# Optimization experiments

Hardware: AMD Instinct MI355X
Metric: run time of the kernel (lower is better)

## Reference

```python
import jax, jax.numpy as jnp
import numpy as np
from jax import lax

B, K, SF, BORDER = 2, 512, 8, 10
H, W = 256, 256
C1, C2 = 64, 128
C = C1 + C2  # feature_channels -> DescMatchingModule in_channels
OUT_CH = 2


def setup_inputs() -> dict:
    key = jax.random.key(0)
    ks = jax.random.split(key, 8)
    return {
        "heatmaps1": jax.random.normal(ks[0], (B, 1, H, W), jnp.float32),
        "heatmaps2": jax.random.normal(ks[1], (B, 1, H, W), jnp.float32),
        "feat1a": jax.random.normal(ks[2], (B, C1, H, W), jnp.float32),
        "feat1b": jax.random.normal(ks[3], (B, C2, H // 2, W // 2), jnp.float32),
        "feat2a": jax.random.normal(ks[4], (B, C1, H, W), jnp.float32),
        "feat2b": jax.random.normal(ks[5], (B, C2, H // 2, W // 2), jnp.float32),
        "fc_w": jax.random.normal(ks[6], (OUT_CH, C), jnp.float32) * np.sqrt(2.0 / C),
        "fc_b": jnp.zeros((OUT_CH,), jnp.float32),
    }


def bilinear_sample(img, gx, gy):
    # img: [b,c,h,w]; gx,gy: [b,k] normalized coords in [-1,1] (align_corners=True)
    b, c, h, w = img.shape
    ix = (gx + 1.0) * 0.5 * (w - 1)
    iy = (gy + 1.0) * 0.5 * (h - 1)
    x0 = jnp.floor(ix); y0 = jnp.floor(iy)
    wx = (ix - x0)[:, None, :]
    wy = (iy - y0)[:, None, :]

    def gather(xx, yy):
        xx = jnp.clip(xx.astype(jnp.int32), 0, w - 1)
        yy = jnp.clip(yy.astype(jnp.int32), 0, h - 1)
        return jax.vmap(lambda im, y_, x_: im[:, y_, x_])(img, yy, xx)  # [b,c,k]

    v00 = gather(x0, y0); v01 = gather(x0 + 1, y0)
    v10 = gather(x0, y0 + 1); v11 = gather(x0 + 1, y0 + 1)
    return (v00 * (1 - wx) * (1 - wy) + v01 * wx * (1 - wy)
            + v10 * (1 - wx) * wy + v11 * wx * wy)  # [b,c,k]


def sampling_layer(heatmap_logits, feats):
    # heatmap_logits: [b,1,H,W]; feats: list of [b,ci,hi,wi]
    b = heatmap_logits.shape[0]
    h = jax.nn.sigmoid(heatmap_logits)
    # max_pool2d + max_unpool2d NMS: keep only window maxima, zero elsewhere
    pooled = lax.reduce_window(h, -jnp.inf, lax.max,
                               (1, 1, SF, SF), (1, 1, SF, SF), 'VALID')
    up = jnp.repeat(jnp.repeat(pooled, SF, axis=2), SF, axis=3)
    nms = jnp.where(h >= up, h, 0.0)
    # border mask
    mask = jnp.zeros((H, W), h.dtype).at[BORDER:H - BORDER, BORDER:W - BORDER].set(1.0)
    nms = nms * mask
    # top-k keypoints by NMS score (training path: always take k points)
    flat = nms.reshape(b, H * W)
    _, idx = lax.top_k(flat, K)            # [b,K]
    row = (idx // W).astype(jnp.float32)   # y (image row)
    col = (idx % W).astype(jnp.float32)    # x (image col)
    gx = 2.0 * col / (W - 1) - 1.0
    gy = 2.0 * row / (H - 1) - 1.0
    pts = jnp.stack([gx, gy], axis=-1)[:, :, None, :]  # [b,K,1,2]
    score = bilinear_sample(h, gx, gy)[:, 0, :]        # [b,K], from sigmoid heatmap
    desc = jnp.concatenate([bilinear_sample(f, gx, gy) for f in feats], axis=1)  # [b,C,K]
    return pts, score, desc


def desc_matching(d1, d2, fc_w, fc_b):
    # d1,d2: [b,C,K] -> [b,K,C]
    o1 = jnp.transpose(d1, (0, 2, 1))
    o2 = jnp.transpose(d2, (0, 2, 1))
    b, k1, c = o1.shape
    k2 = o2.shape[1]
    prod = o1[:, :, None, :] * o2[:, None, :, :]               # [b,k1,k2,C]
    out = prod.reshape(-1, c) @ fc_w.T + fc_b                  # [b*k1*k2, 2]
    n1 = o1 / (1e-6 + jnp.linalg.norm(o1, axis=-1, keepdims=True))
    n2 = o2 / (1e-6 + jnp.linalg.norm(o2, axis=-1, keepdims=True))
    diff = n1[:, :, None, :] - n2[:, None, :, :]
    out_norm = jnp.linalg.norm(diff, axis=-1)                  # [b,k1,k2]
    return out, out_norm


def reference(heatmaps1, heatmaps2, feat1a, feat1b, feat2a, feat2b, fc_w, fc_b):
    lm1, probs1, desc1 = sampling_layer(heatmaps1, [feat1a, feat1b])
    lm2, probs2, desc2 = sampling_layer(heatmaps2, [feat2a, feat2b])
    score, norm = desc_matching(desc1, desc2, fc_w, fc_b)
    return (probs1, probs2, lm1, lm2, score, norm)
```

## Files before the change

kernel.cpp:

```cpp
#include <hip/hip_runtime.h>
#include <hip/hip_bf16.h>
#include <math.h>

#define NPIX 65536

typedef short short8 __attribute__((ext_vector_type(8)));
typedef float f32x4 __attribute__((ext_vector_type(4)));

__device__ int            g_kp_idx[2048];
__device__ float          g_invws[2048];
__device__ float          g_nnws[2048];
__device__ __hip_bfloat16 g_dbf[2048 * 192];
__device__ __hip_bfloat16 g_dw0[1024 * 192];
__device__ __hip_bfloat16 g_dw1[1024 * 192];

__device__ __forceinline__ unsigned long long u64min(unsigned long long a, unsigned long long b) {
    return a < b ? a : b;
}
__device__ __forceinline__ unsigned long long u64max(unsigned long long a, unsigned long long b) {
    return a > b ? a : b;
}

__global__ __launch_bounds__(1024) void nms_topk_kernel(
        const float* __restrict__ hm1, const float* __restrict__ hm2,
        float* __restrict__ out) {
    __shared__ unsigned long long keys[1024];
    int img = blockIdx.x;
    int t = threadIdx.x;
    int b = img & 1, hmid = img >> 1;
    const float* hp = (hmid ? hm2 : hm1) + b * NPIX;

    int wy = t >> 5, wx = t & 31;
    const float* wp = hp + wy * 8 * 256 + wx * 8;
    float mv = -3.4e38f;
    int mi = 0;
    #pragma unroll
    for (int r = 0; r < 8; ++r) {
        float4 v0 = *reinterpret_cast<const float4*>(wp + r * 256);
        float4 v1 = *reinterpret_cast<const float4*>(wp + r * 256 + 4);
        float s[8] = {v0.x, v0.y, v0.z, v0.w, v1.x, v1.y, v1.z, v1.w};
        int rowbase = (wy * 8 + r) * 256 + wx * 8;
        #pragma unroll
        for (int cidx = 0; cidx < 8; ++cidx) {
            if (s[cidx] > mv) { mv = s[cidx]; mi = rowbase + cidx; }
        }
    }
    int ay = mi >> 8, ax = mi & 255;
    bool interior = (ay >= 10 && ay < 246 && ax >= 10 && ax < 246);
    unsigned int ub = __float_as_uint(mv);
    unsigned int mk = (ub & 0x80000000u) ? ~ub : (ub | 0x80000000u);
    if (!interior) mk = 0u;
    unsigned long long k = ((unsigned long long)(~mk) << 32) |
                           (unsigned long long)(unsigned int)mi;

    for (int size = 2; size <= 1024; size <<= 1) {
        for (int stride = size >> 1; stride >= 1; stride >>= 1) {
            bool dir_up = ((t & size) == 0);
            unsigned long long pk;
            if (stride >= 64) {
                __syncthreads();
                keys[t] = k;
                __syncthreads();
                pk = keys[t ^ stride];
            } else {
                pk = __shfl_xor(k, stride);
            }
            bool low = ((t & stride) == 0);
            k = ((low == dir_up)) ? u64min(k, pk) : u64max(k, pk);
        }
    }

    if (t < 512) {
        unsigned int fidx = (unsigned int)(k & 0xFFFFFFFFull);
        unsigned int mk2 = ~(unsigned int)(k >> 32);
        unsigned int lb = (mk2 & 0x80000000u) ? (mk2 ^ 0x80000000u) : ~mk2;
        float logit = __uint_as_float(lb);
        float v = 1.0f / (1.0f + expf(-logit));
        int row = fidx >> 8, col = fidx & 255;
        float gx = 2.0f * (float)col / 255.0f - 1.0f;
        float gy = 2.0f * (float)row / 255.0f - 1.0f;
        out[hmid * 1024 + b * 512 + t] = v;
        float* lm = out + (hmid ? 4096 : 2048) + (size_t)(b * 512 + t) * 2;
        lm[0] = gx; lm[1] = gy;
        g_kp_idx[img * 512 + t] = (int)fidx;
    }
}

__global__ __launch_bounds__(256) void desc_kernel(
        const float* __restrict__ f1a, const float* __restrict__ f1b,
        const float* __restrict__ f2a, const float* __restrict__ f2b,
        const float* __restrict__ fcw) {
    int wave = threadIdx.x >> 6, lane = threadIdx.x & 63;
    int kp = blockIdx.x * 4 + wave;
    int img = kp >> 9, b = img & 1, hmid = img >> 1;
    int fidx = g_kp_idx[kp];
    int row = fidx >> 8, col = fidx & 255;

    const float* fa = (hmid ? f2a : f1a) + (size_t)(b * 64 + lane) * 65536;
    float vfa = fa[fidx];

    float gx = 2.0f * (float)col / 255.0f - 1.0f;
    float gy = 2.0f * (float)row / 255.0f - 1.0f;
    float ix = (gx + 1.0f) * 0.5f * 127.0f;
    float iy = (gy + 1.0f) * 0.5f * 127.0f;
    int x0 = (int)ix, y0 = (int)iy;
    float wx = ix - (float)x0, wy = iy - (float)y0;
    float w00 = (1 - wx) * (1 - wy), w01 = wx * (1 - wy);
    float w10 = (1 - wx) * wy,       w11 = wx * wy;

    const float* fb0 = (hmid ? f2b : f1b) + (size_t)(b * 128 + lane) * 16384
                       + y0 * 128 + x0;
    float vb1 = fb0[0] * w00 + fb0[1] * w01 + fb0[128] * w10 + fb0[129] * w11;
    const float* fb1 = fb0 + (size_t)64 * 16384;
    float vb2 = fb1[0] * w00 + fb1[1] * w01 + fb1[128] * w10 + fb1[129] * w11;

    __hip_bfloat16* dp = g_dbf + (size_t)kp * 192;
    dp[lane]       = __float2bfloat16(vfa);
    dp[lane + 64]  = __float2bfloat16(vb1);
    dp[lane + 128] = __float2bfloat16(vb2);

    if (kp < 1024) {
        __hip_bfloat16* q0 = g_dw0 + (size_t)kp * 192;
        __hip_bfloat16* q1 = g_dw1 + (size_t)kp * 192;
        q0[lane]       = __float2bfloat16(vfa * fcw[lane]);
        q0[lane + 64]  = __float2bfloat16(vb1 * fcw[lane + 64]);
        q0[lane + 128] = __float2bfloat16(vb2 * fcw[lane + 128]);
        q1[lane]       = __float2bfloat16(vfa * fcw[192 + lane]);
        q1[lane + 64]  = __float2bfloat16(vb1 * fcw[192 + lane + 64]);
        q1[lane + 128] = __float2bfloat16(vb2 * fcw[192 + lane + 128]);
    }

    float sq = vfa * vfa + vb1 * vb1 + vb2 * vb2;
    #pragma unroll
    for (int m = 1; m <= 32; m <<= 1) sq += __shfl_xor(sq, m);
    if (lane == 0) {
        float nrm = sqrtf(sq);
        float inv = 1.0f / (1e-6f + nrm);
        g_invws[kp] = inv;
        g_nnws[kp] = sq * inv * inv;
    }
}

__global__ __launch_bounds__(256) void match_kernel(
        const float* __restrict__ fcb, float* __restrict__ out) {
    int t = threadIdx.x;
    int w = t >> 6, lane = t & 63;
    int b = blockIdx.z;
    int k1base = blockIdx.y * 16;
    int k2base = blockIdx.x * 64 + w * 16;
    int r1 = k1base + (lane & 15);
    int r2 = k2base + (lane & 15);
    int koff = (lane >> 4) * 8;

    const __hip_bfloat16* pA  = g_dbf + (size_t)(b * 512 + r1) * 192 + koff;
    const __hip_bfloat16* pW0 = g_dw0 + (size_t)(b * 512 + r1) * 192 + koff;
    const __hip_bfloat16* pW1 = g_dw1 + (size_t)(b * 512 + r1) * 192 + koff;
    const __hip_bfloat16* pB  = g_dbf + (size_t)((2 + b) * 512 + r2) * 192 + koff;

    f32x4 accd = {0.f, 0.f, 0.f, 0.f};
    f32x4 acc0 = {0.f, 0.f, 0.f, 0.f};
    f32x4 acc1 = {0.f, 0.f, 0.f, 0.f};
    #pragma unroll
    for (int kc = 0; kc < 6; ++kc) {
        short8 a  = *reinterpret_cast<const short8*>(pA  + kc * 32);
        short8 a0 = *reinterpret_cast<const short8*>(pW0 + kc * 32);
        short8 a1 = *reinterpret_cast<const short8*>(pW1 + kc * 32);
        short8 bb = *reinterpret_cast<const short8*>(pB  + kc * 32);
        accd = __builtin_amdgcn_mfma_f32_16x16x32_bf16(a,  bb, accd, 0, 0, 0);
        acc0 = __builtin_amdgcn_mfma_f32_16x16x32_bf16(a0, bb, acc0, 0, 0, 0);
        acc1 = __builtin_amdgcn_mfma_f32_16x16x32_bf16(a1, bb, acc1, 0, 0, 0);
    }

    float bb0 = fcb[0], bb1 = fcb[1];
    int col = lane & 15;
    int k2 = k2base + col;
    float inv2 = g_invws[(2 + b) * 512 + k2];
    float nn2  = g_nnws[(2 + b) * 512 + k2];
    #pragma unroll
    for (int j = 0; j < 4; ++j) {
        int k1 = k1base + (lane >> 4) * 4 + j;
        float inv1 = g_invws[b * 512 + k1];
        float nn1  = g_nnws[b * 512 + k1];
        size_t sidx = (size_t)(b * 512 + k1) * 512 + k2;
        float2 sc = make_float2(acc0[j] + bb0, acc1[j] + bb1);
        *reinterpret_cast<float2*>(out + 6144 + sidx * 2) = sc;
        float arg = nn1 + nn2 - 2.0f * inv1 * inv2 * accd[j];
        out[1054720 + sidx] = sqrtf(fmaxf(arg, 0.0f));
    }
}

extern "C" void kernel_launch(void* const* d_in, const int* in_sizes, int n_in,
                              void* d_out, int out_size, void* d_ws, size_t ws_size,
                              hipStream_t stream) {
    const float* hm1 = (const float*)d_in[0];
    const float* hm2 = (const float*)d_in[1];
    const float* f1a = (const float*)d_in[2];
    const float* f1b = (const float*)d_in[3];
    const float* f2a = (const float*)d_in[4];
    const float* f2b = (const float*)d_in[5];
    const float* fcw = (const float*)d_in[6];
    const float* fcb = (const float*)d_in[7];
    float* out = (float*)d_out;
    (void)d_ws; (void)ws_size;

    nms_topk_kernel<<<4, 1024, 0, stream>>>(hm1, hm2, out);
    desc_kernel<<<512, 256, 0, stream>>>(f1a, f1b, f2a, f2b, fcw);
    dim3 g(8, 32, 2);
    match_kernel<<<g, 256, 0, stream>>>(fcb, out);
}
```

Measured before the change: 39.44 us.

## Split NMS window max into wide kernel and spread descriptor sampling across blocks

The window-max step moves out of the four-block top-k kernel into its own 1024-block kernel, with one wave per 8x8 window and a shuffle reduction. The candidates are staged in a global buffer for a separate bitonic top-k kernel. The descriptor kernel now uses one 192-thread block per keypoint, one thread per channel, with a shared-memory partial norm reduction. The goal is more parallelism for the heatmap scan and the gathers, at the cost of an extra kernel launch and a global round trip for the candidates.

```diff
diff --git a/kernel.cpp b/kernel.cpp
--- a/kernel.cpp
+++ b/kernel.cpp
@@ -7,6 +7,7 @@
 typedef short short8 __attribute__((ext_vector_type(8)));
 typedef float f32x4 __attribute__((ext_vector_type(4)));
 
+__device__ unsigned long long g_cand[4096];
 __device__ int            g_kp_idx[2048];
 __device__ float          g_invws[2048];
 __device__ float          g_nnws[2048];
@@ -21,37 +22,43 @@
     return a > b ? a : b;
 }
 
-__global__ __launch_bounds__(1024) void nms_topk_kernel(
-        const float* __restrict__ hm1, const float* __restrict__ hm2,
-        float* __restrict__ out) {
+__global__ __launch_bounds__(256) void winmax_kernel(
+        const float* __restrict__ hm1, const float* __restrict__ hm2) {
+    int wid  = blockIdx.x * 4 + (threadIdx.x >> 6);
+    int lane = threadIdx.x & 63;
+    int img  = wid >> 10;
+    int win  = wid & 1023;
+    int b = img & 1;
+    const float* hp = ((img >> 1) ? hm2 : hm1) + b * NPIX;
+    int wy = win >> 5, wx = win & 31;
+    int py = wy * 8 + (lane >> 3);
+    int px = wx * 8 + (lane & 7);
+    int fidx = py * 256 + px;
+    float mv = hp[fidx];
+    int mi = fidx;
+    #pragma unroll
+    for (int m = 1; m <= 32; m <<= 1) {
+        float ov = __shfl_xor(mv, m);
+        int   oi = __shfl_xor(mi, m);
+        if (ov > mv || (ov == mv && oi < mi)) { mv = ov; mi = oi; }
+    }
+    if (lane == 0) {
+        int ay = mi >> 8, ax = mi & 255;
+        bool interior = (ay >= 10 && ay < 246 && ax >= 10 && ax < 246);
+        unsigned int ub = __float_as_uint(mv);
+        unsigned int mk = (ub & 0x80000000u) ? ~ub : (ub | 0x80000000u);
+        if (!interior) mk = 0u;
+        g_cand[wid] = ((unsigned long long)(~mk) << 32) |
+                      (unsigned long long)(unsigned int)mi;
+    }
+}
+
+__global__ __launch_bounds__(1024) void topk_kernel(float* __restrict__ out) {
     __shared__ unsigned long long keys[1024];
     int img = blockIdx.x;
     int t = threadIdx.x;
     int b = img & 1, hmid = img >> 1;
-    const float* hp = (hmid ? hm2 : hm1) + b * NPIX;
-
-    int wy = t >> 5, wx = t & 31;
-    const float* wp = hp + wy * 8 * 256 + wx * 8;
-    float mv = -3.4e38f;
-    int mi = 0;
-    #pragma unroll
-    for (int r = 0; r < 8; ++r) {
-        float4 v0 = *reinterpret_cast<const float4*>(wp + r * 256);
-        float4 v1 = *reinterpret_cast<const float4*>(wp + r * 256 + 4);
-        float s[8] = {v0.x, v0.y, v0.z, v0.w, v1.x, v1.y, v1.z, v1.w};
-        int rowbase = (wy * 8 + r) * 256 + wx * 8;
-        #pragma unroll
-        for (int cidx = 0; cidx < 8; ++cidx) {
-            if (s[cidx] > mv) { mv = s[cidx]; mi = rowbase + cidx; }
-        }
-    }
-    int ay = mi >> 8, ax = mi & 255;
-    bool interior = (ay >= 10 && ay < 246 && ax >= 10 && ax < 246);
-    unsigned int ub = __float_as_uint(mv);
-    unsigned int mk = (ub & 0x80000000u) ? ~ub : (ub | 0x80000000u);
-    if (!interior) mk = 0u;
-    unsigned long long k = ((unsigned long long)(~mk) << 32) |
-                           (unsigned long long)(unsigned int)mi;
+    unsigned long long k = g_cand[img * 1024 + t];
 
     for (int size = 2; size <= 1024; size <<= 1) {
         for (int stride = size >> 1; stride >= 1; stride >>= 1) {
@@ -86,58 +93,52 @@
     }
 }
 
-__global__ __launch_bounds__(256) void desc_kernel(
+__global__ void desc_kernel(
         const float* __restrict__ f1a, const float* __restrict__ f1b,
         const float* __restrict__ f2a, const float* __restrict__ f2b,
         const float* __restrict__ fcw) {
-    int wave = threadIdx.x >> 6, lane = threadIdx.x & 63;
-    int kp = blockIdx.x * 4 + wave;
+    __shared__ float part[3];
+    int kp = blockIdx.x;
+    int c = threadIdx.x;
     int img = kp >> 9, b = img & 1, hmid = img >> 1;
     int fidx = g_kp_idx[kp];
     int row = fidx >> 8, col = fidx & 255;
 
-    const float* fa = (hmid ? f2a : f1a) + (size_t)(b * 64 + lane) * 65536;
-    float vfa = fa[fidx];
-
-    float gx = 2.0f * (float)col / 255.0f - 1.0f;
-    float gy = 2.0f * (float)row / 255.0f - 1.0f;
-    float ix = (gx + 1.0f) * 0.5f * 127.0f;
-    float iy = (gy + 1.0f) * 0.5f * 127.0f;
-    int x0 = (int)ix, y0 = (int)iy;
-    float wx = ix - (float)x0, wy = iy - (float)y0;
-    float w00 = (1 - wx) * (1 - wy), w01 = wx * (1 - wy);
-    float w10 = (1 - wx) * wy,       w11 = wx * wy;
-
-    const float* fb0 = (hmid ? f2b : f1b) + (size_t)(b * 128 + lane) * 16384
-                       + y0 * 128 + x0;
-    float vb1 = fb0[0] * w00 + fb0[1] * w01 + fb0[128] * w10 + fb0[129] * w11;
-    const float* fb1 = fb0 + (size_t)64 * 16384;
-    float vb2 = fb1[0] * w00 + fb1[1] * w01 + fb1[128] * w10 + fb1[129] * w11;
-
-    __hip_bfloat16* dp = g_dbf + (size_t)kp * 192;
-    dp[lane]       = __float2bfloat16(vfa);
-    dp[lane + 64]  = __float2bfloat16(vb1);
-    dp[lane + 128] = __float2bfloat16(vb2);
-
+    float val;
+    if (c < 64) {
+        const float* fa = (hmid ? f2a : f1a) + (size_t)(b * 64 + c) * 65536;
+        val = fa[fidx];
+    } else {
+        float gx = 2.0f * (float)col / 255.0f - 1.0f;
+        float gy = 2.0f * (float)row / 255.0f - 1.0f;
+        float ix = (gx + 1.0f) * 0.5f * 127.0f;
+        float iy = (gy + 1.0f) * 0.5f * 127.0f;
+        int x0 = (int)ix, y0 = (int)iy;
+        float wx = ix - (float)x0, wy = iy - (float)y0;
+        const float* fb0 = (hmid ? f2b : f1b) + (size_t)(b * 128 + (c - 64)) * 16384
+                           + y0 * 128 + x0;
+        float v00 = fb0[0], v01 = fb0[1], v10 = fb0[128], v11 = fb0[129];
+        val = v00 * (1 - wx) * (1 - wy) + v01 * wx * (1 - wy)
+            + v10 * (1 - wx) * wy       + v11 * wx * wy;
+    }
+
+    g_dbf[(size_t)kp * 192 + c] = __float2bfloat16(val);
     if (kp < 1024) {
-        __hip_bfloat16* q0 = g_dw0 + (size_t)kp * 192;
-        __hip_bfloat16* q1 = g_dw1 + (size_t)kp * 192;
-        q0[lane]       = __float2bfloat16(vfa * fcw[lane]);
-        q0[lane + 64]  = __float2bfloat16(vb1 * fcw[lane + 64]);
-        q0[lane + 128] = __float2bfloat16(vb2 * fcw[lane + 128]);
-        q1[lane]       = __float2bfloat16(vfa * fcw[192 + lane]);
-        q1[lane + 64]  = __float2bfloat16(vb1 * fcw[192 + lane + 64]);
-        q1[lane + 128] = __float2bfloat16(vb2 * fcw[192 + lane + 128]);
-    }
-
-    float sq = vfa * vfa + vb1 * vb1 + vb2 * vb2;
+        g_dw0[(size_t)kp * 192 + c] = __float2bfloat16(val * fcw[c]);
+        g_dw1[(size_t)kp * 192 + c] = __float2bfloat16(val * fcw[192 + c]);
+    }
+
+    float sq = val * val;
     #pragma unroll
     for (int m = 1; m <= 32; m <<= 1) sq += __shfl_xor(sq, m);
-    if (lane == 0) {
-        float nrm = sqrtf(sq);
+    if ((threadIdx.x & 63) == 0) part[threadIdx.x >> 6] = sq;
+    __syncthreads();
+    if (threadIdx.x == 0) {
+        float ss = part[0] + part[1] + part[2];
+        float nrm = sqrtf(ss);
         float inv = 1.0f / (1e-6f + nrm);
         g_invws[kp] = inv;
-        g_nnws[kp] = sq * inv * inv;
+        g_nnws[kp] = ss * inv * inv;
     }
 }
 
@@ -172,8 +173,8 @@
     }
 
     float bb0 = fcb[0], bb1 = fcb[1];
-    int col = lane & 15;
-    int k2 = k2base + col;
+    int colc = lane & 15;
+    int k2 = k2base + colc;
     float inv2 = g_invws[(2 + b) * 512 + k2];
     float nn2  = g_nnws[(2 + b) * 512 + k2];
     #pragma unroll
@@ -203,8 +204,9 @@
     float* out = (float*)d_out;
     (void)d_ws; (void)ws_size;
 
-    nms_topk_kernel<<<4, 1024, 0, stream>>>(hm1, hm2, out);
-    desc_kernel<<<512, 256, 0, stream>>>(f1a, f1b, f2a, f2b, fcw);
+    winmax_kernel<<<1024, 256, 0, stream>>>(hm1, hm2);
+    topk_kernel<<<4, 1024, 0, stream>>>(out);
+    desc_kernel<<<2048, 192, 0, stream>>>(f1a, f1b, f2a, f2b, fcw);
     dim3 g(8, 32, 2);
     match_kernel<<<g, 256, 0, stream>>>(fcb, out);
 }
```

After: 40.93 us. 1.04x slower.

## Stage half-res feature channels in LDS and compute norms in match kernel

Applied to the files above, without the earlier changes.

The descriptor kernel is split into two block roles. Even blocks load one full 128x128 half-resolution channel into shared memory (64 KB) and bilinearly sample all 512 keypoints from it. Odd blocks gather the full-resolution channel values per keypoint. Descriptor norms are no longer computed there: the match kernel recomputes them from the bf16 descriptors into shared memory, so the per-row global norm arrays go away. The aim is to replace scattered per-channel gathers with coalesced streaming loads. The cost is reading whole channels, 64 KB of LDS per block limiting occupancy, and redundant norm work in every match block computed from bf16 rather than fp32 values.

```diff
diff --git a/kernel.cpp b/kernel.cpp
--- a/kernel.cpp
+++ b/kernel.cpp
@@ -8,8 +8,6 @@
 typedef float f32x4 __attribute__((ext_vector_type(4)));
 
 __device__ int            g_kp_idx[2048];
-__device__ float          g_invws[2048];
-__device__ float          g_nnws[2048];
 __device__ __hip_bfloat16 g_dbf[2048 * 192];
 __device__ __hip_bfloat16 g_dw0[1024 * 192];
 __device__ __hip_bfloat16 g_dw1[1024 * 192];
@@ -90,66 +88,112 @@
         const float* __restrict__ f1a, const float* __restrict__ f1b,
         const float* __restrict__ f2a, const float* __restrict__ f2b,
         const float* __restrict__ fcw) {
-    int wave = threadIdx.x >> 6, lane = threadIdx.x & 63;
-    int kp = blockIdx.x * 4 + wave;
-    int img = kp >> 9, b = img & 1, hmid = img >> 1;
-    int fidx = g_kp_idx[kp];
-    int row = fidx >> 8, col = fidx & 255;
-
-    const float* fa = (hmid ? f2a : f1a) + (size_t)(b * 64 + lane) * 65536;
-    float vfa = fa[fidx];
-
-    float gx = 2.0f * (float)col / 255.0f - 1.0f;
-    float gy = 2.0f * (float)row / 255.0f - 1.0f;
-    float ix = (gx + 1.0f) * 0.5f * 127.0f;
-    float iy = (gy + 1.0f) * 0.5f * 127.0f;
-    int x0 = (int)ix, y0 = (int)iy;
-    float wx = ix - (float)x0, wy = iy - (float)y0;
-    float w00 = (1 - wx) * (1 - wy), w01 = wx * (1 - wy);
-    float w10 = (1 - wx) * wy,       w11 = wx * wy;
-
-    const float* fb0 = (hmid ? f2b : f1b) + (size_t)(b * 128 + lane) * 16384
-                       + y0 * 128 + x0;
-    float vb1 = fb0[0] * w00 + fb0[1] * w01 + fb0[128] * w10 + fb0[129] * w11;
-    const float* fb1 = fb0 + (size_t)64 * 16384;
-    float vb2 = fb1[0] * w00 + fb1[1] * w01 + fb1[128] * w10 + fb1[129] * w11;
-
-    __hip_bfloat16* dp = g_dbf + (size_t)kp * 192;
-    dp[lane]       = __float2bfloat16(vfa);
-    dp[lane + 64]  = __float2bfloat16(vb1);
-    dp[lane + 128] = __float2bfloat16(vb2);
-
-    if (kp < 1024) {
-        __hip_bfloat16* q0 = g_dw0 + (size_t)kp * 192;
-        __hip_bfloat16* q1 = g_dw1 + (size_t)kp * 192;
-        q0[lane]       = __float2bfloat16(vfa * fcw[lane]);
-        q0[lane + 64]  = __float2bfloat16(vb1 * fcw[lane + 64]);
-        q0[lane + 128] = __float2bfloat16(vb2 * fcw[lane + 128]);
-        q1[lane]       = __float2bfloat16(vfa * fcw[192 + lane]);
-        q1[lane + 64]  = __float2bfloat16(vb1 * fcw[192 + lane + 64]);
-        q1[lane + 128] = __float2bfloat16(vb2 * fcw[192 + lane + 128]);
-    }
-
-    float sq = vfa * vfa + vb1 * vb1 + vb2 * vb2;
-    #pragma unroll
-    for (int m = 1; m <= 32; m <<= 1) sq += __shfl_xor(sq, m);
-    if (lane == 0) {
-        float nrm = sqrtf(sq);
-        float inv = 1.0f / (1e-6f + nrm);
-        g_invws[kp] = inv;
-        g_nnws[kp] = sq * inv * inv;
+    __shared__ float img_lds[16384];
+    int bid = blockIdx.x;
+    int sub = bid >> 1;
+    int t = threadIdx.x;
+    if ((bid & 1) == 0) {
+        int img = sub >> 7, c = sub & 127;
+        int b = img & 1, hmid = img >> 1;
+        const float4* src = reinterpret_cast<const float4*>(
+            (hmid ? f2b : f1b) + (size_t)(b * 128 + c) * 16384);
+        float4* dst = reinterpret_cast<float4*>(img_lds);
+        #pragma unroll
+        for (int i = 0; i < 16; ++i) dst[t + 256 * i] = src[t + 256 * i];
+        __syncthreads();
+        float w0 = fcw[64 + c], w1 = fcw[192 + 64 + c];
+        #pragma unroll
+        for (int r = 0; r < 2; ++r) {
+            int kpl = t * 2 + r;
+            int kp = img * 512 + kpl;
+            int fidx = g_kp_idx[kp];
+            int row = fidx >> 8, col = fidx & 255;
+            float gx = 2.0f * (float)col / 255.0f - 1.0f;
+            float gy = 2.0f * (float)row / 255.0f - 1.0f;
+            float ix = (gx + 1.0f) * 0.5f * 127.0f;
+            float iy = (gy + 1.0f) * 0.5f * 127.0f;
+            int x0 = (int)ix, y0 = (int)iy;
+            float wx = ix - (float)x0, wy = iy - (float)y0;
+            const float* p = img_lds + y0 * 128 + x0;
+            float val = p[0] * (1 - wx) * (1 - wy) + p[1] * wx * (1 - wy)
+                      + p[128] * (1 - wx) * wy    + p[129] * wx * wy;
+            g_dbf[(size_t)kp * 192 + 64 + c] = __float2bfloat16(val);
+            if (img < 2) {
+                g_dw0[(size_t)kp * 192 + 64 + c] = __float2bfloat16(val * w0);
+                g_dw1[(size_t)kp * 192 + 64 + c] = __float2bfloat16(val * w1);
+            }
+        }
+    } else {
+        int img = sub >> 7, kpg = sub & 127;
+        int b = img & 1, hmid = img >> 1;
+        int kpl = kpg * 4 + (t >> 6);
+        int c = t & 63;
+        int kp = img * 512 + kpl;
+        int fidx = g_kp_idx[kp];
+        const float* fa = (hmid ? f2a : f1a) + (size_t)(b * 64 + c) * 65536;
+        float val = fa[fidx];
+        g_dbf[(size_t)kp * 192 + c] = __float2bfloat16(val);
+        if (img < 2) {
+            g_dw0[(size_t)kp * 192 + c] = __float2bfloat16(val * fcw[c]);
+            g_dw1[(size_t)kp * 192 + c] = __float2bfloat16(val * fcw[192 + c]);
+        }
     }
 }
 
 __global__ __launch_bounds__(256) void match_kernel(
         const float* __restrict__ fcb, float* __restrict__ out) {
+    __shared__ float inv1_s[16], nn1_s[16], inv2_s[64], nn2_s[64];
     int t = threadIdx.x;
     int w = t >> 6, lane = t & 63;
     int b = blockIdx.z;
     int k1base = blockIdx.y * 16;
-    int k2base = blockIdx.x * 64 + w * 16;
+    int k2base = blockIdx.x * 64;
+
+    {
+        int slot = t >> 2, part = t & 3;
+        const __hip_bfloat16* dp = g_dbf +
+            (size_t)((2 + b) * 512 + k2base + slot) * 192 + part * 48;
+        float sq = 0.f;
+        #pragma unroll
+        for (int i = 0; i < 48; ++i) {
+            float v = __bfloat162float(dp[i]);
+            sq += v * v;
+        }
+        sq += __shfl_xor(sq, 1);
+        sq += __shfl_xor(sq, 2);
+        if (part == 0) {
+            float nrm = sqrtf(sq);
+            float inv = 1.0f / (1e-6f + nrm);
+            inv2_s[slot] = inv;
+            nn2_s[slot] = sq * inv * inv;
+        }
+    }
+    {
+        int slot = t >> 4, part = t & 15;
+        const __hip_bfloat16* dp = g_dbf +
+            (size_t)(b * 512 + k1base + slot) * 192 + part * 12;
+        float sq = 0.f;
+        #pragma unroll
+        for (int i = 0; i < 12; ++i) {
+            float v = __bfloat162float(dp[i]);
+            sq += v * v;
+        }
+        sq += __shfl_xor(sq, 1);
+        sq += __shfl_xor(sq, 2);
+        sq += __shfl_xor(sq, 4);
+        sq += __shfl_xor(sq, 8);
+        if (part == 0) {
+            float nrm = sqrtf(sq);
+            float inv = 1.0f / (1e-6f + nrm);
+            inv1_s[slot] = inv;
+            nn1_s[slot] = sq * inv * inv;
+        }
+    }
+    __syncthreads();
+
+    int k2w = k2base + w * 16;
     int r1 = k1base + (lane & 15);
-    int r2 = k2base + (lane & 15);
+    int r2 = k2w + (lane & 15);
     int koff = (lane >> 4) * 8;
 
     const __hip_bfloat16* pA  = g_dbf + (size_t)(b * 512 + r1) * 192 + koff;
@@ -172,15 +216,16 @@
     }
 
     float bb0 = fcb[0], bb1 = fcb[1];
-    int col = lane & 15;
-    int k2 = k2base + col;
-    float inv2 = g_invws[(2 + b) * 512 + k2];
-    float nn2  = g_nnws[(2 + b) * 512 + k2];
+    int colc = lane & 15;
+    int k2 = k2w + colc;
+    float inv2 = inv2_s[w * 16 + colc];
+    float nn2  = nn2_s[w * 16 + colc];
     #pragma unroll
     for (int j = 0; j < 4; ++j) {
-        int k1 = k1base + (lane >> 4) * 4 + j;
-        float inv1 = g_invws[b * 512 + k1];
-        float nn1  = g_nnws[b * 512 + k1];
+        int s1 = (lane >> 4) * 4 + j;
+        int k1 = k1base + s1;
+        float inv1 = inv1_s[s1];
+        float nn1  = nn1_s[s1];
         size_t sidx = (size_t)(b * 512 + k1) * 512 + k2;
         float2 sc = make_float2(acc0[j] + bb0, acc1[j] + bb1);
         *reinterpret_cast<float2*>(out + 6144 + sidx * 2) = sc;
@@ -204,7 +249,7 @@
     (void)d_ws; (void)ws_size;
 
     nms_topk_kernel<<<4, 1024, 0, stream>>>(hm1, hm2, out);
-    desc_kernel<<<512, 256, 0, stream>>>(f1a, f1b, f2a, f2b, fcw);
+    desc_kernel<<<1024, 256, 0, stream>>>(f1a, f1b, f2a, f2b, fcw);
     dim3 g(8, 32, 2);
     match_kernel<<<g, 256, 0, stream>>>(fcb, out);
 }
```

Measured after the change: 42.29 us. +7.2%, slower.
